# Performance work log

Measured on AMD Instinct MI355X. Metric: run time of the kernel, lower is better.

The kernel has to match this reference:

```python
import jax, jax.numpy as jnp
import numpy as np

N, N_SPINS, N_HIDDEN = 8192, 1024, 1024


def setup_inputs() -> dict:
    key = jax.random.key(0)
    ks = jax.random.split(key, 6)
    s_in = 1.0 / np.sqrt(N_SPINS)
    s_h = 1.0 / np.sqrt(N_HIDDEN)
    return {
        "x": jax.random.normal(ks[0], (N, N_SPINS), dtype=jnp.float32),
        "W_in": jax.random.normal(ks[1], (N_HIDDEN, N_SPINS), dtype=jnp.float32) * s_in,
        "b_in": jax.random.normal(ks[2], (N_HIDDEN,), dtype=jnp.float32) * s_in,
        "Wq": jax.random.normal(ks[3], (N_HIDDEN, N_HIDDEN), dtype=jnp.float32) * s_h,
        "Wk": jax.random.normal(ks[4], (N_HIDDEN, N_HIDDEN), dtype=jnp.float32) * s_h,
        "Wv": jax.random.normal(ks[5], (N_HIDDEN, N_HIDDEN), dtype=jnp.float32) * s_h,
    }


def reference(x, W_in, b_in, Wq, Wk, Wv):
    # embedding: Linear(n_spins, n_hidden)  -> h: [N, H]
    h = x @ W_in.T + b_in
    q = h @ Wq.T                      # [N, H]
    k = h @ Wk.T                      # [N, H]
    v = h @ Wv.T                      # [N, H]
    scores = (q @ k.T) * 0.25         # [N, N], scale 1/4 as in source
    attn = jax.nn.softmax(scores, axis=0)  # softmax over dim=0 (columns)
    out = attn @ v                    # [N, H]
    # log(cosh(z)) = |z| + log1p(exp(-2|z|)) - log(2), numerically stable
    a = jnp.abs(out)
    logcosh = a + jnp.log1p(jnp.exp(-2.0 * a)) - jnp.log(jnp.asarray(2.0, out.dtype))
    return jnp.sum(logcosh, axis=-1)  # [N]
```

## Files before the change

### kernel.cpp

```cpp
#include <hip/hip_runtime.h>
#include <hip/hip_bf16.h>
#include <cstdint>
#include <cstddef>

#define NTOK 8192
#define NHID 1024

typedef __attribute__((ext_vector_type(8))) __bf16 bf16x8;
typedef __attribute__((ext_vector_type(4))) float f32x4;

__device__ __forceinline__ unsigned short f2bf(float f) {
    union { float f; unsigned u; } v; v.f = f;
    unsigned r = v.u + 0x7FFF + ((v.u >> 16) & 1);
    return (unsigned short)(r >> 16);
}

__device__ __forceinline__ float bf2f(unsigned short u) {
    union { unsigned u; float f; } v; v.u = ((unsigned)u) << 16;
    return v.f;
}

__device__ __forceinline__ void async_copy16(const void* gsrc, void* ldsdst) {
    __builtin_amdgcn_global_load_lds(
        (const __attribute__((address_space(1))) unsigned int*)gsrc,
        (__attribute__((address_space(3))) unsigned int*)ldsdst,
        16, 0, 0);
}

template <int EPI, bool SWAP>
__global__ __launch_bounds__(256) void gemm_bt(
    const unsigned short* __restrict__ A,
    const unsigned short* __restrict__ B,
    void* __restrict__ C,
    const float* __restrict__ bias,
    float* __restrict__ zsum,
    float scale, int M, int N, int K, int lda, int ldb)
{
    __shared__ __attribute__((aligned(16))) unsigned short As[128 * 64];
    __shared__ __attribute__((aligned(16))) unsigned short Bs[128 * 64];

    const int tid  = threadIdx.x;
    const int wave = tid >> 6;
    const int lane = tid & 63;
    const int bm = (SWAP ? blockIdx.x : blockIdx.y) * 128;
    const int bn = (SWAP ? blockIdx.y : blockIdx.x) * 128;
    const size_t ldaz = (size_t)lda;
    const size_t ldbz = (size_t)ldb;

    const int srow = lane >> 3;
    const int scol = ((lane & 7) ^ srow) * 8;
    const unsigned short* Ag[4];
    const unsigned short* Bg[4];
    unsigned short* Al[4];
    unsigned short* Bl[4];
#pragma unroll
    for (int t = 0; t < 4; ++t) {
        int r = (wave * 4 + t) * 8 + srow;
        Ag[t] = A + (size_t)(bm + r) * ldaz + scol;
        Bg[t] = B + (size_t)(bn + r) * ldbz + scol;
        Al[t] = &As[(wave * 4 + t) * 512];
        Bl[t] = &Bs[(wave * 4 + t) * 512];
    }

    const int wm = (wave >> 1) * 64;
    const int wn = (wave & 1) * 64;
    const int fr = lane & 15;
    const int frl = fr & 7;
    const int q = lane >> 4;

    f32x4 acc[4][4] = {};

    for (int kt = 0; kt < K; kt += 64) {
#pragma unroll
        for (int t = 0; t < 4; ++t) {
            async_copy16(Ag[t], Al[t]);
            async_copy16(Bg[t], Bl[t]);
            Ag[t] += 64;
            Bg[t] += 64;
        }
        __syncthreads();
#pragma unroll
        for (int ks = 0; ks < 2; ++ks) {
            const int pc = ((ks * 4 + q) ^ frl) * 8;
            bf16x8 a[4], b[4];
#pragma unroll
            for (int i = 0; i < 4; ++i) {
                a[i] = *(const bf16x8*)&As[(wm + i * 16 + fr) * 64 + pc];
                b[i] = *(const bf16x8*)&Bs[(wn + i * 16 + fr) * 64 + pc];
            }
#pragma unroll
            for (int i = 0; i < 4; ++i)
#pragma unroll
                for (int j = 0; j < 4; ++j)
                    acc[i][j] = __builtin_amdgcn_mfma_f32_16x16x32_bf16(
                        a[i], b[j], acc[i][j], 0, 0, 0);
        }
        __syncthreads();
    }

    const int erow = q * 4;
#pragma unroll
    for (int j = 0; j < 4; ++j) {
        const int gcol = bn + wn + j * 16 + fr;
        const float bv = (EPI != 2 && bias) ? bias[gcol] : 0.0f;
        float colsum = 0.0f;
#pragma unroll
        for (int i = 0; i < 4; ++i) {
            const int grow0 = bm + wm + i * 16 + erow;
#pragma unroll
            for (int r = 0; r < 4; ++r) {
                float v;
                if (EPI == 2) {
                    v = __expf(fmaf(acc[i][j][r], scale, -64.0f));
                    colsum += v;
                } else {
                    v = acc[i][j][r] * scale + bv;
                }
                size_t idx = (size_t)(grow0 + r) * N + gcol;
                if (EPI == 0) ((float*)C)[idx] = v;
                else          ((unsigned short*)C)[idx] = f2bf(v);
            }
        }
        if (EPI == 2) {
            colsum += __shfl_xor(colsum, 16, 64);
            colsum += __shfl_xor(colsum, 32, 64);
            if (q == 0) atomicAdd(&zsum[gcol], colsum);
        }
    }
}

__global__ void cvt_all(const float4* __restrict__ x,
                        const float4* __restrict__ w0,
                        const float4* __restrict__ w1,
                        const float4* __restrict__ w2,
                        const float4* __restrict__ w3,
                        ushort4* __restrict__ xb,
                        ushort4* __restrict__ wdst,
                        int n4x, int n4w)
{
    int i = blockIdx.x * blockDim.x + threadIdx.x;
    float4 f;
    ushort4* dst;
    if (i < n4x) {
        f = x[i]; dst = xb + i;
    } else {
        int r = i - n4x;
        int seg = r / n4w, off = r % n4w;
        const float4* src = (seg == 0) ? w0 : (seg == 1) ? w1 : (seg == 2) ? w2 : w3;
        f = src[off]; dst = wdst + r;
    }
    ushort4 o;
    o.x = f2bf(f.x); o.y = f2bf(f.y); o.z = f2bf(f.z); o.w = f2bf(f.w);
    *dst = o;
}

__global__ void vt_scale(uint4* __restrict__ vt8,
                         const float* __restrict__ z)
{
    int idx = blockIdx.x * blockDim.x + threadIdx.x;
    int jj = (idx & (NTOK / 8 - 1)) * 8;
    uint4 v = vt8[idx];
    unsigned short* vp = (unsigned short*)&v;
    float4 z0 = *(const float4*)&z[jj];
    float4 z1 = *(const float4*)&z[jj + 4];
    uint4 o;
    unsigned short* op = (unsigned short*)&o;
    op[0] = f2bf(bf2f(vp[0]) / z0.x);
    op[1] = f2bf(bf2f(vp[1]) / z0.y);
    op[2] = f2bf(bf2f(vp[2]) / z0.z);
    op[3] = f2bf(bf2f(vp[3]) / z0.w);
    op[4] = f2bf(bf2f(vp[4]) / z1.x);
    op[5] = f2bf(bf2f(vp[5]) / z1.y);
    op[6] = f2bf(bf2f(vp[6]) / z1.z);
    op[7] = f2bf(bf2f(vp[7]) / z1.w);
    vt8[idx] = o;
}

__global__ void logcosh_rowsum(const ushort4* __restrict__ O4,
                               float* __restrict__ out)
{
    const float LN2 = 0.69314718055994531f;
    int row = blockIdx.x;
    ushort4 u = O4[(size_t)row * 256 + threadIdx.x];
    float s = 0.0f, a;
    a = fabsf(bf2f(u.x)); s += a + log1pf(__expf(-2.0f * a));
    a = fabsf(bf2f(u.y)); s += a + log1pf(__expf(-2.0f * a));
    a = fabsf(bf2f(u.z)); s += a + log1pf(__expf(-2.0f * a));
    a = fabsf(bf2f(u.w)); s += a + log1pf(__expf(-2.0f * a));
    s -= 4.0f * LN2;
    for (int off = 32; off; off >>= 1) s += __shfl_down(s, off, 64);
    __shared__ float red[4];
    if ((threadIdx.x & 63) == 0) red[threadIdx.x >> 6] = s;
    __syncthreads();
    if (threadIdx.x == 0) out[row] = red[0] + red[1] + red[2] + red[3];
}

extern "C" void kernel_launch(void* const* d_in, const int* in_sizes, int n_in,
                              void* d_out, int out_size, void* d_ws, size_t ws_size,
                              hipStream_t stream)
{
    (void)in_sizes; (void)n_in; (void)out_size; (void)ws_size;

    const float* x    = (const float*)d_in[0];
    const float* W_in = (const float*)d_in[1];
    const float* b_in = (const float*)d_in[2];
    const float* Wq   = (const float*)d_in[3];
    const float* Wk   = (const float*)d_in[4];
    const float* Wv   = (const float*)d_in[5];
    float* out = (float*)d_out;

    char* w = (char*)d_ws;
    const size_t MiB = 1024 * 1024;
    unsigned short* Pb     = (unsigned short*)(w);
    unsigned short* xb     = (unsigned short*)(w + 128 * MiB);
    unsigned short* vtb    = (unsigned short*)(w + 128 * MiB);
    unsigned short* hb     = (unsigned short*)(w + 144 * MiB);
    unsigned short* qk     = (unsigned short*)(w + 160 * MiB);
    unsigned short* outb   = (unsigned short*)(w + 160 * MiB);
    unsigned short* wib    = (unsigned short*)(w + 192 * MiB);
    unsigned short* wqkb   = (unsigned short*)(w + 194 * MiB);
    unsigned short* wvb    = (unsigned short*)(w + 198 * MiB);
    float*          pz     = (float*)         (w + 200 * MiB);

    {
        int n4x = NTOK * NHID / 4;
        int n4w = NHID * NHID / 4;
        int n4  = n4x + 4 * n4w;
        cvt_all<<<(n4 + 255) / 256, 256, 0, stream>>>(
            (const float4*)x, (const float4*)W_in, (const float4*)Wq,
            (const float4*)Wk, (const float4*)Wv,
            (ushort4*)xb, (ushort4*)wib, n4x, n4w);
        hipMemsetAsync(pz, 0, NTOK * sizeof(float), stream);
    }

    dim3 gNH(NHID / 128, NTOK / 128);
    gemm_bt<1, false><<<gNH, 256, 0, stream>>>(
        xb, wib, hb, b_in, nullptr, 1.0f, NTOK, NHID, NHID, NHID, NHID);

    dim3 gQK(2 * NHID / 128, NTOK / 128);
    gemm_bt<1, false><<<gQK, 256, 0, stream>>>(
        hb, wqkb, qk, nullptr, nullptr, 1.0f, NTOK, 2 * NHID, NHID, NHID, NHID);

    dim3 gVT(NTOK / 128, NHID / 128);
    gemm_bt<1, false><<<gVT, 256, 0, stream>>>(
        wvb, hb, vtb, nullptr, nullptr, 1.0f, NHID, NTOK, NHID, NHID, NHID);

    dim3 gS(NTOK / 128, NTOK / 128);
    gemm_bt<2, false><<<gS, 256, 0, stream>>>(
        qk, qk + NHID, Pb, nullptr, pz, 0.25f, NTOK, NTOK, NHID, 2 * NHID, 2 * NHID);

    vt_scale<<<(NHID * NTOK / 8) / 256, 256, 0, stream>>>((uint4*)vtb, pz);

    dim3 gO(NTOK / 128, NHID / 128);
    gemm_bt<1, true><<<gO, 256, 0, stream>>>(
        Pb, vtb, outb, nullptr, nullptr, 1.0f, NTOK, NHID, NTOK, NTOK, NTOK);

    logcosh_rowsum<<<NTOK, 256, 0, stream>>>((const ushort4*)outb, out);
}
```

Before: 548.8 us.

## Fuse Q/K/V projections into one GEMM and transpose V with scaling

Merges the separate QK and transposed-V GEMMs into a single QKV GEMM over the concatenated weights, writing a [N,3H] buffer. A new LDS-tiled transpose_scale kernel then transposes V and divides by the column softmax sums, replacing the in-place vt_scale pass. The memset of the sum buffer is folded into the conversion kernel, which removes a separate launch. The trade is an extra explicit transpose pass over V in exchange for one larger GEMM with better occupancy, plus a rearranged workspace layout.

```diff
diff --git a/kernel.cpp b/kernel.cpp
--- a/kernel.cpp
+++ b/kernel.cpp
@@ -102,7 +102,7 @@
 #pragma unroll
     for (int j = 0; j < 4; ++j) {
         const int gcol = bn + wn + j * 16 + fr;
-        const float bv = (EPI != 2 && bias) ? bias[gcol] : 0.0f;
+        const float bv = (EPI == 1 && bias) ? bias[gcol] : 0.0f;
         float colsum = 0.0f;
 #pragma unroll
         for (int i = 0; i < 4; ++i) {
@@ -136,9 +136,16 @@
                         const float4* __restrict__ w3,
                         ushort4* __restrict__ xb,
                         ushort4* __restrict__ wdst,
+                        float4* __restrict__ pz4,
                         int n4x, int n4w)
 {
     int i = blockIdx.x * blockDim.x + threadIdx.x;
+    int n4 = n4x + 4 * n4w;
+    if (i >= n4) {
+        int zi = i - n4;
+        if (zi < 2048) pz4[zi] = make_float4(0.f, 0.f, 0.f, 0.f);
+        return;
+    }
     float4 f;
     ushort4* dst;
     if (i < n4x) {
@@ -154,26 +161,29 @@
     *dst = o;
 }
 
-__global__ void vt_scale(uint4* __restrict__ vt8,
-                         const float* __restrict__ z)
-{
-    int idx = blockIdx.x * blockDim.x + threadIdx.x;
-    int jj = (idx & (NTOK / 8 - 1)) * 8;
-    uint4 v = vt8[idx];
-    unsigned short* vp = (unsigned short*)&v;
-    float4 z0 = *(const float4*)&z[jj];
-    float4 z1 = *(const float4*)&z[jj + 4];
-    uint4 o;
-    unsigned short* op = (unsigned short*)&o;
-    op[0] = f2bf(bf2f(vp[0]) / z0.x);
-    op[1] = f2bf(bf2f(vp[1]) / z0.y);
-    op[2] = f2bf(bf2f(vp[2]) / z0.z);
-    op[3] = f2bf(bf2f(vp[3]) / z0.w);
-    op[4] = f2bf(bf2f(vp[4]) / z1.x);
-    op[5] = f2bf(bf2f(vp[5]) / z1.y);
-    op[6] = f2bf(bf2f(vp[6]) / z1.z);
-    op[7] = f2bf(bf2f(vp[7]) / z1.w);
-    vt8[idx] = o;
+__global__ __launch_bounds__(256) void transpose_scale(
+    const unsigned short* __restrict__ v,
+    const float* __restrict__ z,
+    unsigned short* __restrict__ vt)
+{
+    __shared__ float lds[64 * 65];
+    const int tid = threadIdx.x;
+    const int j0 = blockIdx.x * 64;
+    const int h0 = blockIdx.y * 64;
+    const int c = tid & 63;
+    const int r0 = tid >> 6;
+#pragma unroll
+    for (int it = 0; it < 16; ++it) {
+        int r = it * 4 + r0;
+        lds[r * 65 + c] = bf2f(v[(size_t)(j0 + r) * 3072 + h0 + c]);
+    }
+    __syncthreads();
+    const float rz = 1.0f / z[j0 + c];
+#pragma unroll
+    for (int it = 0; it < 16; ++it) {
+        int r = it * 4 + r0;
+        vt[(size_t)(h0 + r) * NTOK + j0 + c] = f2bf(lds[c * 65 + r] * rz);
+    }
 }
 
 __global__ void logcosh_rowsum(const ushort4* __restrict__ O4,
@@ -212,44 +222,40 @@
     char* w = (char*)d_ws;
     const size_t MiB = 1024 * 1024;
     unsigned short* Pb     = (unsigned short*)(w);
+    unsigned short* qkv    = (unsigned short*)(w + 128 * MiB);
     unsigned short* xb     = (unsigned short*)(w + 128 * MiB);
-    unsigned short* vtb    = (unsigned short*)(w + 128 * MiB);
-    unsigned short* hb     = (unsigned short*)(w + 144 * MiB);
-    unsigned short* qk     = (unsigned short*)(w + 160 * MiB);
-    unsigned short* outb   = (unsigned short*)(w + 160 * MiB);
+    unsigned short* outb   = (unsigned short*)(w + 128 * MiB);
+    unsigned short* hb     = (unsigned short*)(w + 176 * MiB);
+    unsigned short* vtb    = (unsigned short*)(w + 176 * MiB);
     unsigned short* wib    = (unsigned short*)(w + 192 * MiB);
-    unsigned short* wqkb   = (unsigned short*)(w + 194 * MiB);
-    unsigned short* wvb    = (unsigned short*)(w + 198 * MiB);
+    unsigned short* wqkvb  = (unsigned short*)(w + 194 * MiB);
     float*          pz     = (float*)         (w + 200 * MiB);
 
     {
         int n4x = NTOK * NHID / 4;
         int n4w = NHID * NHID / 4;
         int n4  = n4x + 4 * n4w;
-        cvt_all<<<(n4 + 255) / 256, 256, 0, stream>>>(
+        cvt_all<<<n4 / 256 + 8, 256, 0, stream>>>(
             (const float4*)x, (const float4*)W_in, (const float4*)Wq,
             (const float4*)Wk, (const float4*)Wv,
-            (ushort4*)xb, (ushort4*)wib, n4x, n4w);
-        hipMemsetAsync(pz, 0, NTOK * sizeof(float), stream);
+            (ushort4*)xb, (ushort4*)wib, (float4*)pz, n4x, n4w);
     }
 
     dim3 gNH(NHID / 128, NTOK / 128);
     gemm_bt<1, false><<<gNH, 256, 0, stream>>>(
         xb, wib, hb, b_in, nullptr, 1.0f, NTOK, NHID, NHID, NHID, NHID);
 
-    dim3 gQK(2 * NHID / 128, NTOK / 128);
-    gemm_bt<1, false><<<gQK, 256, 0, stream>>>(
-        hb, wqkb, qk, nullptr, nullptr, 1.0f, NTOK, 2 * NHID, NHID, NHID, NHID);
-
-    dim3 gVT(NTOK / 128, NHID / 128);
-    gemm_bt<1, false><<<gVT, 256, 0, stream>>>(
-        wvb, hb, vtb, nullptr, nullptr, 1.0f, NHID, NTOK, NHID, NHID, NHID);
+    dim3 gQKV(3 * NHID / 128, NTOK / 128);
+    gemm_bt<1, false><<<gQKV, 256, 0, stream>>>(
+        hb, wqkvb, qkv, nullptr, nullptr, 1.0f, NTOK, 3 * NHID, NHID, NHID, NHID);
 
     dim3 gS(NTOK / 128, NTOK / 128);
     gemm_bt<2, false><<<gS, 256, 0, stream>>>(
-        qk, qk + NHID, Pb, nullptr, pz, 0.25f, NTOK, NTOK, NHID, 2 * NHID, 2 * NHID);
-
-    vt_scale<<<(NHID * NTOK / 8) / 256, 256, 0, stream>>>((uint4*)vtb, pz);
+        qkv, qkv + NHID, Pb, nullptr, pz, 0.25f, NTOK, NTOK, NHID,
+        3 * NHID, 3 * NHID);
+
+    dim3 gT(NTOK / 64, NHID / 64);
+    transpose_scale<<<gT, 256, 0, stream>>>(qkv + 2 * NHID, pz, vtb);
 
     dim3 gO(NTOK / 128, NHID / 128);
     gemm_bt<1, true><<<gO, 256, 0, stream>>>(
```

Result: faster. 534.7 us, median of 2 (-2.6%).
